# Kernel optimization log

Measured on AMD Instinct MI355X. Metric: run time of the kernel, lower is better.

## Reference

```python
import jax, jax.numpy as jnp
import numpy as np

H, W, C = 1080, 1920, 3


def setup_inputs() -> dict:
    key = jax.random.key(0)
    k1, k2, k3 = jax.random.split(key, 3)
    img = jax.random.normal(k1, (H, W, C), dtype=jnp.float32)
    # ~10px typical displacement for realistic optical flow
    flow = jax.random.normal(k2, (1, H, W, 2), dtype=jnp.float32) * 10.0
    # depths in [0.1, 80); no pixel hits the 100.0 invalid sentinel
    depth = jax.random.uniform(k3, (H, W), dtype=jnp.float32, minval=0.1, maxval=80.0)
    return {"img": img, "flow": flow, "depth": depth, "split": 10}


def reference(img, flow, depth, split):
    # Depth-ordered forward-warping splat (z-buffer style compositing).
    # kernel_size=1 -> nearest-neighbor splat: each source pixel (y,x) writes
    # its value to (round(y+flow_y), round(x+flow_x)); passes go far->near and
    # nearer (nonzero) writes overwrite farther ones.
    flow = flow[0]                      # [H, W, 2], (dx, dy)
    h, w, c = img.shape

    # midpoints of the depth histogram, excluding the 100.0 invalid sentinel
    valid = depth != 100.0
    sd = jnp.sort(jnp.where(valid, depth, jnp.inf).ravel())
    l = valid.sum()
    step = l // split
    mids = jnp.concatenate(
        [jnp.take(sd, jnp.arange(split) * step), jnp.take(sd, l - 1)[None]]
    )  # [split+1], ascending

    ys, xs = jnp.meshgrid(jnp.arange(h), jnp.arange(w), indexing="ij")
    ty = jnp.round(ys + flow[..., 1]).astype(jnp.int32)   # target row
    tx = jnp.round(xs + flow[..., 0]).astype(jnp.int32)   # target col

    res = jnp.zeros_like(img)
    for i in range(split, 0, -1):       # far bin first, near bin last
        dmask = (depth < mids[i]) & (depth >= mids[i - 1])   # [H, W]
        # pixels outside the bin scatter to row h -> dropped (mode='drop')
        ty_i = jnp.where(dmask, ty, h)
        out = jnp.zeros_like(img).at[ty_i, tx].set(
            img * dmask[..., None].astype(img.dtype), mode="drop"
        )
        # nearer nonzero splats overwrite; zeros keep previous content
        res = res * (out == 0) + out
    return res
```

## Files before the change

### kernel.cpp

```cpp
#include <hip/hip_runtime.h>

typedef unsigned int u32;

static constexpr int HH = 1080, WW = 1920;
static constexpr int NPIX = HH * WW;
static constexpr int NQ = 17;
static constexpr int MAXOWN = 16;
static constexpr int OPB = 4;
static constexpr int NGRP = MAXOWN / OPB;
static constexpr int NBLK = 512;
static constexpr int BT   = 1024;
static constexpr int R1 = 16;
static constexpr int NCH1 = 64;
static constexpr int TS = 64;
static constexpr int TCX = WW / TS;
static constexpr int TCY = (HH + TS - 1) / TS;
static constexpr int NTILE = TCX * TCY;
static constexpr int NT512 = 512;

static constexpr size_t MIDS_OFF  = 0;
static constexpr size_t QB1_OFF   = 128;
static constexpr size_t QR1_OFF   = 256;
static constexpr size_t OIDX_OFF  = 384;
static constexpr size_t OBIN_OFF  = 512;
static constexpr size_t NOWN_OFF  = 640;
static constexpr size_t KEY22_OFF = 768;
static constexpr size_t R2O_OFF   = 896;
static constexpr size_t TOT1_OFF  = 1024;
static constexpr size_t GH2_OFF   = TOT1_OFF + (size_t)R1 * 4096 * 4;
static constexpr size_t ZERO_BYTES = GH2_OFF + (size_t)NQ * 1024 * 4;
static constexpr size_t TCNT_OFF  = ZERO_BYTES;
static constexpr size_t TTOT_OFF  = TCNT_OFF + (size_t)NBLK * NT512 * 4;
static constexpr size_t TBASE_OFF = TTOT_OFF + NT512 * 4;
static constexpr size_t TEND_OFF  = TBASE_OFF + NT512 * 4;
static constexpr size_t BASE2_OFF = TEND_OFF + NT512 * 4;
static constexpr size_t GH1_OFF   = BASE2_OFF + (size_t)NBLK * NT512 * 4;
static constexpr size_t PAIRS_OFF = GH1_OFF + (size_t)MAXOWN * NCH1 * 1024 * 4;

__device__ __forceinline__ int target_of(int y, int x, float fx, float fy) {
    int ty = (int)rintf((float)y + fy);
    int tx = (int)rintf((float)x + fx);
    if (ty < 0) ty += HH;
    if (tx < 0) tx += WW;
    if ((unsigned)ty >= (unsigned)HH || (unsigned)tx >= (unsigned)WW) return -1;
    return ty * WW + tx;
}

__global__ __launch_bounds__(BT) void k_histA_cnt(const float* __restrict__ depth,
                                                  const float* __restrict__ flow,
                                                  u32* __restrict__ tot1,
                                                  u32* __restrict__ tcnt) {
    __shared__ u32 h[4096];
    __shared__ u32 tc[NT512];
    int tid = threadIdx.x;
    for (int j = tid; j < 4096; j += BT) h[j] = 0;
    for (int j = tid; j < NT512; j += BT) tc[j] = 0;
    __syncthreads();
    const int nvec = NPIX / 4;
    for (int v = blockIdx.x * BT + tid; v < nvec; v += gridDim.x * BT) {
        int i = v * 4;
        float4 d4 = ((const float4*)depth)[v];
        float4 fa = ((const float4*)flow)[v * 2];
        float4 fb = ((const float4*)flow)[v * 2 + 1];
        int y = i / WW, x0 = i - y * WW;
        float dd[4] = {d4.x, d4.y, d4.z, d4.w};
        float fx[4] = {fa.x, fa.z, fb.x, fb.z};
        float fy[4] = {fa.y, fa.w, fb.y, fb.w};
        #pragma unroll
        for (int j = 0; j < 4; ++j) {
            if (dd[j] != 100.0f)
                atomicAdd(&h[__float_as_uint(dd[j]) >> 20], 1u);
            int t = target_of(y, x0 + j, fx[j], fy[j]);
            if (t >= 0) {
                int ty = t / WW, tx = t - ty * WW;
                atomicAdd(&tc[(ty >> 6) * TCX + (tx >> 6)], 1u);
            }
        }
    }
    __syncthreads();
    u32 rep = blockIdx.x & (R1 - 1);
    for (int j = tid; j < 4096; j += BT) {
        u32 v = h[j];
        if (v) atomicAdd(&tot1[rep * 4096 + j], v);
    }
    for (int j = tid; j < NT512; j += BT)
        tcnt[blockIdx.x * NT512 + j] = tc[j];
}

__global__ __launch_bounds__(NBLK) void k_tscan(const u32* __restrict__ tcnt,
                                                u32* __restrict__ ttot,
                                                u32* __restrict__ base2) {
    __shared__ u32 s[NBLK];
    int t = blockIdx.x, b = threadIdx.x;
    u32 v = tcnt[b * NT512 + t];
    s[b] = v;
    __syncthreads();
    for (int off = 1; off < NBLK; off <<= 1) {
        u32 x = (b >= off) ? s[b - off] : 0;
        __syncthreads();
        s[b] += x;
        __syncthreads();
    }
    base2[b * NT512 + t] = s[b] - v;
    if (b == NBLK - 1) ttot[t] = s[NBLK - 1];
}

__global__ __launch_bounds__(1024) void k_selA(const u32* __restrict__ tot1,
                                               const int* __restrict__ splitp,
                                               const u32* __restrict__ ttot,
                                               u32* __restrict__ qb1, u32* __restrict__ qr1,
                                               u32* __restrict__ oidx, u32* __restrict__ obin,
                                               u32* __restrict__ nown,
                                               u32* __restrict__ tbase, u32* __restrict__ tend) {
    __shared__ u32 part[1024];
    __shared__ u32 qbS[NQ], qcS[NQ];
    __shared__ u32 totalsh;
    int tid = threadIdx.x;
    int split = *splitp;
    int base = tid * 4;
    u32 cc[4] = {0, 0, 0, 0};
    for (int r = 0; r < R1; ++r)
        for (int j = 0; j < 4; ++j) cc[j] += tot1[r * 4096 + base + j];
    u32 local = cc[0] + cc[1] + cc[2] + cc[3];
    part[tid] = local;
    __syncthreads();
    for (int off = 1; off < 1024; off <<= 1) {
        u32 v = (tid >= off) ? part[tid - off] : 0;
        __syncthreads();
        part[tid] += v;
        __syncthreads();
    }
    if (tid == 1023) totalsh = part[1023];
    __syncthreads();
    u32 l = totalsh;
    u32 step = l / (u32)split;
    u32 cum = part[tid] - local;
    for (int j = 0; j < 4; ++j) {
        u32 c = cc[j];
        if (c) {
            for (int q = 0; q <= split; ++q) {
                u32 r = (q < split) ? (u32)q * step : l - 1u;
                if (r >= cum && r < cum + c) {
                    qb1[q] = (u32)(base + j);
                    qr1[q] = r - cum;
                    qbS[q] = (u32)(base + j);
                    qcS[q] = c;
                }
            }
        }
        cum += c;
    }
    __syncthreads();
    if (tid == 0) {
        int w = -1;
        u32 prev = 0xFFFFFFFFu;
        for (int q = 0; q <= split; ++q) {
            if (qbS[q] != prev) { ++w; prev = qbS[q]; obin[w] = qbS[q]; }
            oidx[q] = (u32)w;
        }
        for (int w2 = w + 1; w2 < MAXOWN; ++w2) obin[w2] = 0xFFFFFFFFu;
        *nown = (u32)(w + 1);
    }
    __syncthreads();
    u32 tv = (tid < NT512) ? ttot[tid] : 0;
    part[tid] = tv;
    __syncthreads();
    for (int off = 1; off < 1024; off <<= 1) {
        u32 v = (tid >= off) ? part[tid - off] : 0;
        __syncthreads();
        part[tid] += v;
        __syncthreads();
    }
    if (tid < NT512) {
        tbase[tid] = part[tid] - tv;
        tend[tid]  = part[tid];
    }
}

__global__ __launch_bounds__(1024) void k_ph1(const float* __restrict__ depth,
                                              const u32* __restrict__ obin,
                                              const u32* __restrict__ nownp,
                                              u32* __restrict__ ghist) {
    int c = blockIdx.x / NGRP;
    int g = blockIdx.x % NGRP;
    int w0 = g * OPB;
    int nown = (int)*nownp;
    if (w0 >= nown) return;
    __shared__ u32 h[OPB * 1024];
    int tid = threadIdx.x;
    u32 ob[OPB];
    #pragma unroll
    for (int k = 0; k < OPB; ++k)
        ob[k] = (w0 + k < nown) ? obin[w0 + k] : 0xFFFFFFFFu;
    for (int j = tid; j < OPB * 1024; j += 1024) h[j] = 0;
    __syncthreads();
    const int per = (NPIX / 4) / NCH1;
    int lo = c * per, hi = lo + per;
    for (int v = lo + tid; v < hi; v += 1024) {
        float4 d4 = ((const float4*)depth)[v];
        float dd[4] = {d4.x, d4.y, d4.z, d4.w};
        #pragma unroll
        for (int j = 0; j < 4; ++j) {
            u32 bits = __float_as_uint(dd[j]);
            u32 b1 = bits >> 20;
            #pragma unroll
            for (int k = 0; k < OPB; ++k)
                if (ob[k] == b1)
                    atomicAdd(&h[k * 1024 + ((bits >> 10) & 1023u)], 1u);
        }
    }
    __syncthreads();
    for (int j = tid; j < OPB * 1024; j += 1024) {
        int k = j >> 10, bin = j & 1023;
        int w = w0 + k;
        if (w < nown) ghist[(w * NCH1 + c) * 1024 + bin] = h[j];
    }
}

__global__ __launch_bounds__(1024) void k_red1(const int* __restrict__ splitp,
                                               const u32* __restrict__ qb1,
                                               const u32* __restrict__ qr1,
                                               const u32* __restrict__ oidx,
                                               const u32* __restrict__ ghist,
                                               u32* __restrict__ key22, u32* __restrict__ r2o) {
    int q = blockIdx.x;
    if (q > *splitp) return;
    int w = (int)oidx[q];
    __shared__ u32 part[1024];
    int tid = threadIdx.x;
    u32 local = 0;
    for (int c = 0; c < NCH1; ++c) local += ghist[(w * NCH1 + c) * 1024 + tid];
    part[tid] = local;
    __syncthreads();
    for (int off = 1; off < 1024; off <<= 1) {
        u32 v = (tid >= off) ? part[tid - off] : 0;
        __syncthreads();
        part[tid] += v;
        __syncthreads();
    }
    u32 target = qr1[q];
    u32 cum = part[tid] - local;
    if (local && target >= cum && target < cum + local) {
        key22[q] = (qb1[q] << 10) | (u32)tid;
        r2o[q] = target - cum;
    }
}

__global__ __launch_bounds__(256) void k_ph2(const float* __restrict__ depth,
                                             const int* __restrict__ splitp,
                                             const u32* __restrict__ key22,
                                             u32* __restrict__ gh2) {
    __shared__ u32 k22[NQ];
    int tid = threadIdx.x, split = *splitp;
    if (tid < NQ) k22[tid] = (tid <= split) ? key22[tid] : 0xFFFFFFFFu;
    __syncthreads();
    const int nvec = NPIX / 4;
    for (int v = blockIdx.x * blockDim.x + tid; v < nvec; v += gridDim.x * blockDim.x) {
        float4 d4 = ((const float4*)depth)[v];
        float dd[4] = {d4.x, d4.y, d4.z, d4.w};
        #pragma unroll
        for (int j = 0; j < 4; ++j) {
            if (dd[j] != 100.0f) {
                u32 bits = __float_as_uint(dd[j]);
                u32 hi22 = bits >> 10;
                for (int q = 0; q <= split; ++q)
                    if (k22[q] == hi22) atomicAdd(&gh2[q * 1024 + (bits & 1023u)], 1u);
            }
        }
    }
}

__global__ __launch_bounds__(1024) void k_red2(const int* __restrict__ splitp,
                                               const u32* __restrict__ key22,
                                               const u32* __restrict__ r2o,
                                               const u32* __restrict__ gh2,
                                               float* __restrict__ mids) {
    int q = blockIdx.x;
    if (q > *splitp) return;
    __shared__ u32 part[1024];
    int tid = threadIdx.x;
    u32 local = gh2[q * 1024 + tid];
    part[tid] = local;
    __syncthreads();
    for (int off = 1; off < 1024; off <<= 1) {
        u32 v = (tid >= off) ? part[tid - off] : 0;
        __syncthreads();
        part[tid] += v;
        __syncthreads();
    }
    u32 target = r2o[q];
    u32 cum = part[tid] - local;
    if (local && target >= cum && target < cum + local)
        mids[q] = __uint_as_float((key22[q] << 10) | (u32)tid);
}

__global__ __launch_bounds__(BT) void k_scatter(const float* __restrict__ depth,
                                                const float* __restrict__ flow,
                                                const int* __restrict__ splitp,
                                                const float* __restrict__ mids,
                                                const u32* __restrict__ tbase,
                                                const u32* __restrict__ base2,
                                                uint2* __restrict__ pairs) {
    __shared__ u32 cur[NT512];
    __shared__ float msh[NQ];
    int tid = threadIdx.x, split = *splitp;
    if (tid < NQ) msh[tid] = (tid <= split) ? mids[tid] : 0.f;
    for (int j = tid; j < NT512; j += BT)
        cur[j] = tbase[j] + base2[blockIdx.x * NT512 + j];
    __syncthreads();
    const int nvec = NPIX / 4;
    for (int v = blockIdx.x * BT + tid; v < nvec; v += gridDim.x * BT) {
        int i = v * 4;
        float4 d4 = ((const float4*)depth)[v];
        float4 fa = ((const float4*)flow)[v * 2];
        float4 fb = ((const float4*)flow)[v * 2 + 1];
        int y = i / WW, x0 = i - y * WW;
        float dd[4] = {d4.x, d4.y, d4.z, d4.w};
        float fx[4] = {fa.x, fa.z, fb.x, fb.z};
        float fy[4] = {fa.y, fa.w, fb.y, fb.w};
        #pragma unroll
        for (int j = 0; j < 4; ++j) {
            int t = target_of(y, x0 + j, fx[j], fy[j]);
            if (t < 0) continue;
            float d = dd[j];
            int rank = -1;
            for (int k = 1; k <= split; ++k)
                if (d >= msh[k - 1] && d < msh[k]) { rank = split - k; break; }
            u32 p = (rank >= 0) ? (u32)rank * (u32)NPIX + (u32)(i + j) + 1u : 0u;
            int ty = t / WW, tx = t - ty * WW;
            int tile = (ty >> 6) * TCX + (tx >> 6);
            u32 pos = atomicAdd(&cur[tile], 1u);
            pairs[pos] = make_uint2((u32)t, p);
        }
    }
}

__global__ __launch_bounds__(1024) void k_tile_reduce(const uint2* __restrict__ pairs,
                                                      const u32* __restrict__ tbase,
                                                      const u32* __restrict__ tend,
                                                      const float* __restrict__ img,
                                                      float* __restrict__ out) {
    __shared__ u32 zb[TS * TS];
    int tid = threadIdx.x;
    int tile = blockIdx.x;
    for (int c = tid; c < TS * TS; c += 1024) zb[c] = 0;
    __syncthreads();
    int ty0 = (tile / TCX) << 6, tx0 = (tile % TCX) << 6;
    u32 b = tbase[tile], e = tend[tile];
    for (u32 k = b + tid; k < e; k += 1024) {
        uint2 pr = pairs[k];
        int t = (int)pr.x;
        int ty = t / WW, tx = t - ty * WW;
        atomicMax(&zb[((ty - ty0) << 6) | (tx - tx0)], pr.y);
    }
    __syncthreads();
    for (int c = tid; c < TS * TS; c += 1024) {
        int ty = ty0 + (c >> 6);
        if (ty >= HH) continue;
        int tx = tx0 + (c & 63);
        u32 p = zb[c];
        float r = 0.f, g = 0.f, bl = 0.f;
        if (p) {
            u32 src = (p - 1u) % (u32)NPIX;
            r  = img[src * 3 + 0];
            g  = img[src * 3 + 1];
            bl = img[src * 3 + 2];
        }
        int t = ty * WW + tx;
        out[t * 3 + 0] = r;
        out[t * 3 + 1] = g;
        out[t * 3 + 2] = bl;
    }
}

extern "C" void kernel_launch(void* const* d_in, const int* in_sizes, int n_in,
                              void* d_out, int out_size, void* d_ws, size_t ws_size,
                              hipStream_t stream) {
    const float* img    = (const float*)d_in[0];
    const float* flow   = (const float*)d_in[1];
    const float* depth  = (const float*)d_in[2];
    const int*   splitp = (const int*)d_in[3];

    char* ws = (char*)d_ws;
    float* mids  = (float*)(ws + MIDS_OFF);
    u32*   qb1   = (u32*)(ws + QB1_OFF);
    u32*   qr1   = (u32*)(ws + QR1_OFF);
    u32*   oidx  = (u32*)(ws + OIDX_OFF);
    u32*   obin  = (u32*)(ws + OBIN_OFF);
    u32*   nown  = (u32*)(ws + NOWN_OFF);
    u32*   key22 = (u32*)(ws + KEY22_OFF);
    u32*   r2o   = (u32*)(ws + R2O_OFF);
    u32*   tot1  = (u32*)(ws + TOT1_OFF);
    u32*   gh2   = (u32*)(ws + GH2_OFF);
    u32*   tcnt  = (u32*)(ws + TCNT_OFF);
    u32*   ttot  = (u32*)(ws + TTOT_OFF);
    u32*   tbase = (u32*)(ws + TBASE_OFF);
    u32*   tend  = (u32*)(ws + TEND_OFF);
    u32*   base2 = (u32*)(ws + BASE2_OFF);
    u32*   gh1   = (u32*)(ws + GH1_OFF);
    uint2* pairs = (uint2*)(ws + PAIRS_OFF);
    float* out   = (float*)d_out;

    hipMemsetAsync(d_ws, 0, ZERO_BYTES, stream);

    k_histA_cnt  <<<NBLK, BT, 0, stream>>>(depth, flow, tot1, tcnt);
    k_tscan      <<<NT512, NBLK, 0, stream>>>(tcnt, ttot, base2);
    k_selA       <<<1, 1024, 0, stream>>>(tot1, splitp, ttot, qb1, qr1, oidx, obin, nown, tbase, tend);
    k_ph1        <<<NCH1 * NGRP, 1024, 0, stream>>>(depth, obin, nown, gh1);
    k_red1       <<<NQ, 1024, 0, stream>>>(splitp, qb1, qr1, oidx, gh1, key22, r2o);
    k_ph2        <<<2048, 256, 0, stream>>>(depth, splitp, key22, gh2);
    k_red2       <<<NQ, 1024, 0, stream>>>(splitp, key22, r2o, gh2, mids);
    k_scatter    <<<NBLK, BT, 0, stream>>>(depth, flow, splitp, mids, tbase, base2, pairs);
    k_tile_reduce<<<NTILE, 1024, 0, stream>>>(pairs, tbase, tend, img, out);
}
```

Measured before the change: 96.92 us.

## Fuse quantile selection kernels into one cooperative kernel with grid syncs

Replaces the memset and seven small launches (histogram, tile scan, selection, two-level radix refinement) with a single cooperative kernel of 256 blocks using grid.sync between phases. It also halves the block count for the tile-count and scatter decomposition to 256 contiguous chunks. The aim is to remove launch gaps and serialization overhead between many tiny kernels. In exchange, parallelism in each phase is capped at 256x512 threads, grid-wide barriers add their own cost, and phases such as the single-block selection run while the rest of the grid idles.

```diff
diff --git a/kernel.cpp b/kernel.cpp
--- a/kernel.cpp
+++ b/kernel.cpp
@@ -1,21 +1,24 @@
 #include <hip/hip_runtime.h>
-
+#include <hip/hip_cooperative_groups.h>
+
+namespace cg = cooperative_groups;
 typedef unsigned int u32;
 
 static constexpr int HH = 1080, WW = 1920;
 static constexpr int NPIX = HH * WW;
+static constexpr int NVEC = NPIX / 4;
 static constexpr int NQ = 17;
 static constexpr int MAXOWN = 16;
+static constexpr int NBC = 256;
+static constexpr int BTC = 512;
+static constexpr int CHUNK = NVEC / NBC;
+static constexpr int R1 = 16;
 static constexpr int OPB = 4;
-static constexpr int NGRP = MAXOWN / OPB;
-static constexpr int NBLK = 512;
-static constexpr int BT   = 1024;
-static constexpr int R1 = 16;
 static constexpr int NCH1 = 64;
+static constexpr int CH1V = NVEC / NCH1;
 static constexpr int TS = 64;
 static constexpr int TCX = WW / TS;
-static constexpr int TCY = (HH + TS - 1) / TS;
-static constexpr int NTILE = TCX * TCY;
+static constexpr int NTILE = 510;
 static constexpr int NT512 = 512;
 
 static constexpr size_t MIDS_OFF  = 0;
@@ -26,15 +29,15 @@
 static constexpr size_t NOWN_OFF  = 640;
 static constexpr size_t KEY22_OFF = 768;
 static constexpr size_t R2O_OFF   = 896;
-static constexpr size_t TOT1_OFF  = 1024;
+static constexpr size_t TTOT_OFF  = 1024;
+static constexpr size_t TBASE_OFF = 3072;
+static constexpr size_t TEND_OFF  = 5120;
+static constexpr size_t TOT1_OFF  = 8192;
 static constexpr size_t GH2_OFF   = TOT1_OFF + (size_t)R1 * 4096 * 4;
-static constexpr size_t ZERO_BYTES = GH2_OFF + (size_t)NQ * 1024 * 4;
-static constexpr size_t TCNT_OFF  = ZERO_BYTES;
-static constexpr size_t TTOT_OFF  = TCNT_OFF + (size_t)NBLK * NT512 * 4;
-static constexpr size_t TBASE_OFF = TTOT_OFF + NT512 * 4;
-static constexpr size_t TEND_OFF  = TBASE_OFF + NT512 * 4;
-static constexpr size_t BASE2_OFF = TEND_OFF + NT512 * 4;
-static constexpr size_t GH1_OFF   = BASE2_OFF + (size_t)NBLK * NT512 * 4;
+static constexpr size_t ZCNT      = (R1 * 4096 + NQ * 1024);
+static constexpr size_t TCNT_OFF  = GH2_OFF + (size_t)NQ * 1024 * 4;
+static constexpr size_t BASE2_OFF = TCNT_OFF + (size_t)NBC * NT512 * 4;
+static constexpr size_t GH1_OFF   = BASE2_OFF + (size_t)NBC * NT512 * 4;
 static constexpr size_t PAIRS_OFF = GH1_OFF + (size_t)MAXOWN * NCH1 * 1024 * 4;
 
 __device__ __forceinline__ int target_of(int y, int x, float fx, float fy) {
@@ -46,270 +49,286 @@
     return ty * WW + tx;
 }
 
-__global__ __launch_bounds__(BT) void k_histA_cnt(const float* __restrict__ depth,
-                                                  const float* __restrict__ flow,
-                                                  u32* __restrict__ tot1,
-                                                  u32* __restrict__ tcnt) {
-    __shared__ u32 h[4096];
-    __shared__ u32 tc[NT512];
-    int tid = threadIdx.x;
-    for (int j = tid; j < 4096; j += BT) h[j] = 0;
-    for (int j = tid; j < NT512; j += BT) tc[j] = 0;
-    __syncthreads();
-    const int nvec = NPIX / 4;
-    for (int v = blockIdx.x * BT + tid; v < nvec; v += gridDim.x * BT) {
-        int i = v * 4;
-        float4 d4 = ((const float4*)depth)[v];
-        float4 fa = ((const float4*)flow)[v * 2];
-        float4 fb = ((const float4*)flow)[v * 2 + 1];
-        int y = i / WW, x0 = i - y * WW;
-        float dd[4] = {d4.x, d4.y, d4.z, d4.w};
-        float fx[4] = {fa.x, fa.z, fb.x, fb.z};
-        float fy[4] = {fa.y, fa.w, fb.y, fb.w};
+__global__ __launch_bounds__(BTC) void k_quant(const float* __restrict__ depth,
+                                               const float* __restrict__ flow,
+                                               const int* __restrict__ splitp,
+                                               char* __restrict__ ws) {
+    cg::grid_group grid = cg::this_grid();
+    __shared__ u32 SM[4608];
+    __shared__ u32 SMQ[40];
+
+    float* mids  = (float*)(ws + MIDS_OFF);
+    u32* qb1   = (u32*)(ws + QB1_OFF);
+    u32* qr1   = (u32*)(ws + QR1_OFF);
+    u32* oidx  = (u32*)(ws + OIDX_OFF);
+    u32* obin  = (u32*)(ws + OBIN_OFF);
+    u32* nown  = (u32*)(ws + NOWN_OFF);
+    u32* key22 = (u32*)(ws + KEY22_OFF);
+    u32* r2o   = (u32*)(ws + R2O_OFF);
+    u32* ttot  = (u32*)(ws + TTOT_OFF);
+    u32* tbase = (u32*)(ws + TBASE_OFF);
+    u32* tend  = (u32*)(ws + TEND_OFF);
+    u32* tot1  = (u32*)(ws + TOT1_OFF);
+    u32* gh2   = (u32*)(ws + GH2_OFF);
+    u32* tcnt  = (u32*)(ws + TCNT_OFF);
+    u32* base2 = (u32*)(ws + BASE2_OFF);
+    u32* gh1   = (u32*)(ws + GH1_OFF);
+
+    const int b = blockIdx.x, tid = threadIdx.x;
+    const int split = *splitp;
+
+    {
+        u32* z = tot1;
+        for (int j = b * BTC + tid; j < (int)ZCNT; j += NBC * BTC) z[j] = 0;
+    }
+    grid.sync();
+
+    {
+        u32* h  = SM;
+        u32* tc = SM + 4096;
+        for (int j = tid; j < 4096; j += BTC) h[j] = 0;
+        tc[tid] = 0;
+        __syncthreads();
+        int lo = b * CHUNK;
+        for (int v = lo + tid; v < lo + CHUNK; v += BTC) {
+            int i = v * 4;
+            float4 d4 = ((const float4*)depth)[v];
+            float4 fa = ((const float4*)flow)[v * 2];
+            float4 fb = ((const float4*)flow)[v * 2 + 1];
+            int y = i / WW, x0 = i - y * WW;
+            float dd[4] = {d4.x, d4.y, d4.z, d4.w};
+            float fx[4] = {fa.x, fa.z, fb.x, fb.z};
+            float fy[4] = {fa.y, fa.w, fb.y, fb.w};
+            #pragma unroll
+            for (int j = 0; j < 4; ++j) {
+                if (dd[j] != 100.0f)
+                    atomicAdd(&h[__float_as_uint(dd[j]) >> 20], 1u);
+                int t = target_of(y, x0 + j, fx[j], fy[j]);
+                if (t >= 0) {
+                    int ty = t / WW, tx = t - ty * WW;
+                    atomicAdd(&tc[(ty >> 6) * TCX + (tx >> 6)], 1u);
+                }
+            }
+        }
+        __syncthreads();
+        u32 rep = (u32)(b & (R1 - 1));
+        for (int j = tid; j < 4096; j += BTC) {
+            u32 v = h[j];
+            if (v) atomicAdd(&tot1[rep * 4096 + j], v);
+        }
+        tcnt[b * NT512 + tid] = tc[tid];
+    }
+    grid.sync();
+
+    {
+        int j = tid & 255, half = tid >> 8;
+        int t = 2 * b + half;
+        u32 val = tcnt[j * NT512 + t];
+        u32* s = SM;
+        s[tid] = val;
+        __syncthreads();
+        for (int off = 1; off < 256; off <<= 1) {
+            u32 x = (j >= off) ? s[tid - off] : 0;
+            __syncthreads();
+            s[tid] += x;
+            __syncthreads();
+        }
+        base2[j * NT512 + t] = s[tid] - val;
+        if (j == 255) ttot[t] = s[tid];
+    }
+    if (b == 0) {
+        __syncthreads();
+        u32* part = SM;
+        u32* qbS  = SMQ;
+        int base = tid * 8;
+        u32 cc[8];
         #pragma unroll
-        for (int j = 0; j < 4; ++j) {
-            if (dd[j] != 100.0f)
-                atomicAdd(&h[__float_as_uint(dd[j]) >> 20], 1u);
-            int t = target_of(y, x0 + j, fx[j], fy[j]);
-            if (t >= 0) {
-                int ty = t / WW, tx = t - ty * WW;
-                atomicAdd(&tc[(ty >> 6) * TCX + (tx >> 6)], 1u);
-            }
-        }
-    }
-    __syncthreads();
-    u32 rep = blockIdx.x & (R1 - 1);
-    for (int j = tid; j < 4096; j += BT) {
-        u32 v = h[j];
-        if (v) atomicAdd(&tot1[rep * 4096 + j], v);
-    }
-    for (int j = tid; j < NT512; j += BT)
-        tcnt[blockIdx.x * NT512 + j] = tc[j];
-}
-
-__global__ __launch_bounds__(NBLK) void k_tscan(const u32* __restrict__ tcnt,
-                                                u32* __restrict__ ttot,
-                                                u32* __restrict__ base2) {
-    __shared__ u32 s[NBLK];
-    int t = blockIdx.x, b = threadIdx.x;
-    u32 v = tcnt[b * NT512 + t];
-    s[b] = v;
-    __syncthreads();
-    for (int off = 1; off < NBLK; off <<= 1) {
-        u32 x = (b >= off) ? s[b - off] : 0;
-        __syncthreads();
-        s[b] += x;
-        __syncthreads();
-    }
-    base2[b * NT512 + t] = s[b] - v;
-    if (b == NBLK - 1) ttot[t] = s[NBLK - 1];
-}
-
-__global__ __launch_bounds__(1024) void k_selA(const u32* __restrict__ tot1,
-                                               const int* __restrict__ splitp,
-                                               const u32* __restrict__ ttot,
-                                               u32* __restrict__ qb1, u32* __restrict__ qr1,
-                                               u32* __restrict__ oidx, u32* __restrict__ obin,
-                                               u32* __restrict__ nown,
-                                               u32* __restrict__ tbase, u32* __restrict__ tend) {
-    __shared__ u32 part[1024];
-    __shared__ u32 qbS[NQ], qcS[NQ];
-    __shared__ u32 totalsh;
-    int tid = threadIdx.x;
-    int split = *splitp;
-    int base = tid * 4;
-    u32 cc[4] = {0, 0, 0, 0};
-    for (int r = 0; r < R1; ++r)
-        for (int j = 0; j < 4; ++j) cc[j] += tot1[r * 4096 + base + j];
-    u32 local = cc[0] + cc[1] + cc[2] + cc[3];
-    part[tid] = local;
-    __syncthreads();
-    for (int off = 1; off < 1024; off <<= 1) {
-        u32 v = (tid >= off) ? part[tid - off] : 0;
-        __syncthreads();
-        part[tid] += v;
-        __syncthreads();
-    }
-    if (tid == 1023) totalsh = part[1023];
-    __syncthreads();
-    u32 l = totalsh;
-    u32 step = l / (u32)split;
-    u32 cum = part[tid] - local;
-    for (int j = 0; j < 4; ++j) {
-        u32 c = cc[j];
-        if (c) {
+        for (int k = 0; k < 8; ++k) cc[k] = 0;
+        for (int r = 0; r < R1; ++r) {
+            const u32* tp = tot1 + r * 4096 + base;
+            #pragma unroll
+            for (int k = 0; k < 8; ++k) cc[k] += tp[k];
+        }
+        u32 local = 0;
+        #pragma unroll
+        for (int k = 0; k < 8; ++k) local += cc[k];
+        part[tid] = local;
+        __syncthreads();
+        for (int off = 1; off < BTC; off <<= 1) {
+            u32 x = (tid >= off) ? part[tid - off] : 0;
+            __syncthreads();
+            part[tid] += x;
+            __syncthreads();
+        }
+        if (tid == BTC - 1) SMQ[32] = part[BTC - 1];
+        __syncthreads();
+        u32 l = SMQ[32];
+        u32 step = l / (u32)split;
+        u32 cum = part[tid] - local;
+        for (int k = 0; k < 8; ++k) {
+            u32 c = cc[k];
+            if (c) {
+                for (int q = 0; q <= split; ++q) {
+                    u32 r = (q < split) ? (u32)q * step : l - 1u;
+                    if (r >= cum && r < cum + c) {
+                        qb1[q] = (u32)(base + k);
+                        qr1[q] = r - cum;
+                        qbS[q] = (u32)(base + k);
+                    }
+                }
+            }
+            cum += c;
+        }
+        __syncthreads();
+        if (tid == 0) {
+            int w = -1;
+            u32 prev = 0xFFFFFFFFu;
             for (int q = 0; q <= split; ++q) {
-                u32 r = (q < split) ? (u32)q * step : l - 1u;
-                if (r >= cum && r < cum + c) {
-                    qb1[q] = (u32)(base + j);
-                    qr1[q] = r - cum;
-                    qbS[q] = (u32)(base + j);
-                    qcS[q] = c;
-                }
-            }
-        }
-        cum += c;
-    }
-    __syncthreads();
-    if (tid == 0) {
-        int w = -1;
-        u32 prev = 0xFFFFFFFFu;
-        for (int q = 0; q <= split; ++q) {
-            if (qbS[q] != prev) { ++w; prev = qbS[q]; obin[w] = qbS[q]; }
-            oidx[q] = (u32)w;
-        }
-        for (int w2 = w + 1; w2 < MAXOWN; ++w2) obin[w2] = 0xFFFFFFFFu;
-        *nown = (u32)(w + 1);
-    }
-    __syncthreads();
-    u32 tv = (tid < NT512) ? ttot[tid] : 0;
-    part[tid] = tv;
-    __syncthreads();
-    for (int off = 1; off < 1024; off <<= 1) {
-        u32 v = (tid >= off) ? part[tid - off] : 0;
-        __syncthreads();
-        part[tid] += v;
-        __syncthreads();
-    }
-    if (tid < NT512) {
-        tbase[tid] = part[tid] - tv;
-        tend[tid]  = part[tid];
-    }
-}
-
-__global__ __launch_bounds__(1024) void k_ph1(const float* __restrict__ depth,
-                                              const u32* __restrict__ obin,
-                                              const u32* __restrict__ nownp,
-                                              u32* __restrict__ ghist) {
-    int c = blockIdx.x / NGRP;
-    int g = blockIdx.x % NGRP;
-    int w0 = g * OPB;
-    int nown = (int)*nownp;
-    if (w0 >= nown) return;
-    __shared__ u32 h[OPB * 1024];
-    int tid = threadIdx.x;
-    u32 ob[OPB];
-    #pragma unroll
-    for (int k = 0; k < OPB; ++k)
-        ob[k] = (w0 + k < nown) ? obin[w0 + k] : 0xFFFFFFFFu;
-    for (int j = tid; j < OPB * 1024; j += 1024) h[j] = 0;
-    __syncthreads();
-    const int per = (NPIX / 4) / NCH1;
-    int lo = c * per, hi = lo + per;
-    for (int v = lo + tid; v < hi; v += 1024) {
-        float4 d4 = ((const float4*)depth)[v];
-        float dd[4] = {d4.x, d4.y, d4.z, d4.w};
-        #pragma unroll
-        for (int j = 0; j < 4; ++j) {
-            u32 bits = __float_as_uint(dd[j]);
-            u32 b1 = bits >> 20;
+                if (qbS[q] != prev) { ++w; prev = qbS[q]; obin[w] = qbS[q]; }
+                oidx[q] = (u32)w;
+            }
+            for (int w2 = w + 1; w2 < MAXOWN; ++w2) obin[w2] = 0xFFFFFFFFu;
+            *nown = (u32)(w + 1);
+        }
+    }
+    grid.sync();
+
+    {
+        int c2 = b >> 2, g = b & 3, w0 = g * OPB;
+        int nw = (int)*nown;
+        if (w0 < nw) {
+            u32 ob[OPB];
             #pragma unroll
             for (int k = 0; k < OPB; ++k)
-                if (ob[k] == b1)
-                    atomicAdd(&h[k * 1024 + ((bits >> 10) & 1023u)], 1u);
-        }
-    }
-    __syncthreads();
-    for (int j = tid; j < OPB * 1024; j += 1024) {
-        int k = j >> 10, bin = j & 1023;
-        int w = w0 + k;
-        if (w < nown) ghist[(w * NCH1 + c) * 1024 + bin] = h[j];
+                ob[k] = (w0 + k < nw) ? obin[w0 + k] : 0xFFFFFFFFu;
+            u32* h = SM;
+            for (int j = tid; j < 4096; j += BTC) h[j] = 0;
+            __syncthreads();
+            int lo = c2 * CH1V;
+            for (int v = lo + tid; v < lo + CH1V; v += BTC) {
+                float4 d4 = ((const float4*)depth)[v];
+                float dd[4] = {d4.x, d4.y, d4.z, d4.w};
+                #pragma unroll
+                for (int j = 0; j < 4; ++j) {
+                    u32 bits = __float_as_uint(dd[j]);
+                    u32 b1 = bits >> 20;
+                    #pragma unroll
+                    for (int k = 0; k < OPB; ++k)
+                        if (ob[k] == b1)
+                            atomicAdd(&h[k * 1024 + ((bits >> 10) & 1023u)], 1u);
+                }
+            }
+            __syncthreads();
+            for (int j = tid; j < 4096; j += BTC) {
+                int k = j >> 10, w = w0 + k;
+                if (w < nw) gh1[(w * NCH1 + c2) * 1024 + (j & 1023)] = SM[j];
+            }
+        }
+        if (b == NBC - 1) {
+            __syncthreads();
+            u32* s = SM;
+            u32 tv = ttot[tid];
+            s[tid] = tv;
+            __syncthreads();
+            for (int off = 1; off < BTC; off <<= 1) {
+                u32 x = (tid >= off) ? s[tid - off] : 0;
+                __syncthreads();
+                s[tid] += x;
+                __syncthreads();
+            }
+            tbase[tid] = s[tid] - tv;
+            tend[tid]  = s[tid];
+        }
+    }
+    grid.sync();
+
+    if (b <= split) {
+        int w = (int)oidx[b];
+        u32 l0 = 0, l1 = 0;
+        for (int c = 0; c < NCH1; ++c) {
+            const u32* gp = gh1 + (size_t)(w * NCH1 + c) * 1024 + 2 * tid;
+            l0 += gp[0];
+            l1 += gp[1];
+        }
+        u32* part = SM;
+        u32 loc = l0 + l1;
+        part[tid] = loc;
+        __syncthreads();
+        for (int off = 1; off < BTC; off <<= 1) {
+            u32 x = (tid >= off) ? part[tid - off] : 0;
+            __syncthreads();
+            part[tid] += x;
+            __syncthreads();
+        }
+        u32 target = qr1[b];
+        u32 cum = part[tid] - loc;
+        if (l0 && target >= cum && target < cum + l0) {
+            key22[b] = (qb1[b] << 10) | (u32)(2 * tid);
+            r2o[b] = target - cum;
+        } else if (l1 && target >= cum + l0 && target < cum + loc) {
+            key22[b] = (qb1[b] << 10) | (u32)(2 * tid + 1);
+            r2o[b] = target - cum - l0;
+        }
+    }
+    grid.sync();
+
+    {
+        u32* k22 = SMQ;
+        if (tid < NQ) k22[tid] = (tid <= split) ? key22[tid] : 0xFFFFFFFFu;
+        __syncthreads();
+        int lo = b * CHUNK;
+        for (int v = lo + tid; v < lo + CHUNK; v += BTC) {
+            float4 d4 = ((const float4*)depth)[v];
+            float dd[4] = {d4.x, d4.y, d4.z, d4.w};
+            #pragma unroll
+            for (int j = 0; j < 4; ++j) {
+                if (dd[j] != 100.0f) {
+                    u32 bits = __float_as_uint(dd[j]);
+                    u32 hi22 = bits >> 10;
+                    for (int q = 0; q <= split; ++q)
+                        if (k22[q] == hi22) atomicAdd(&gh2[q * 1024 + (bits & 1023u)], 1u);
+                }
+            }
+        }
+    }
+    grid.sync();
+
+    if (b <= split) {
+        u32 l0 = gh2[b * 1024 + 2 * tid], l1 = gh2[b * 1024 + 2 * tid + 1];
+        u32* part = SM;
+        u32 loc = l0 + l1;
+        part[tid] = loc;
+        __syncthreads();
+        for (int off = 1; off < BTC; off <<= 1) {
+            u32 x = (tid >= off) ? part[tid - off] : 0;
+            __syncthreads();
+            part[tid] += x;
+            __syncthreads();
+        }
+        u32 target = r2o[b];
+        u32 cum = part[tid] - loc;
+        if (l0 && target >= cum && target < cum + l0)
+            mids[b] = __uint_as_float((key22[b] << 10) | (u32)(2 * tid));
+        else if (l1 && target >= cum + l0 && target < cum + loc)
+            mids[b] = __uint_as_float((key22[b] << 10) | (u32)(2 * tid + 1));
     }
 }
 
-__global__ __launch_bounds__(1024) void k_red1(const int* __restrict__ splitp,
-                                               const u32* __restrict__ qb1,
-                                               const u32* __restrict__ qr1,
-                                               const u32* __restrict__ oidx,
-                                               const u32* __restrict__ ghist,
-                                               u32* __restrict__ key22, u32* __restrict__ r2o) {
-    int q = blockIdx.x;
-    if (q > *splitp) return;
-    int w = (int)oidx[q];
-    __shared__ u32 part[1024];
-    int tid = threadIdx.x;
-    u32 local = 0;
-    for (int c = 0; c < NCH1; ++c) local += ghist[(w * NCH1 + c) * 1024 + tid];
-    part[tid] = local;
-    __syncthreads();
-    for (int off = 1; off < 1024; off <<= 1) {
-        u32 v = (tid >= off) ? part[tid - off] : 0;
-        __syncthreads();
-        part[tid] += v;
-        __syncthreads();
-    }
-    u32 target = qr1[q];
-    u32 cum = part[tid] - local;
-    if (local && target >= cum && target < cum + local) {
-        key22[q] = (qb1[q] << 10) | (u32)tid;
-        r2o[q] = target - cum;
-    }
-}
-
-__global__ __launch_bounds__(256) void k_ph2(const float* __restrict__ depth,
-                                             const int* __restrict__ splitp,
-                                             const u32* __restrict__ key22,
-                                             u32* __restrict__ gh2) {
-    __shared__ u32 k22[NQ];
-    int tid = threadIdx.x, split = *splitp;
-    if (tid < NQ) k22[tid] = (tid <= split) ? key22[tid] : 0xFFFFFFFFu;
-    __syncthreads();
-    const int nvec = NPIX / 4;
-    for (int v = blockIdx.x * blockDim.x + tid; v < nvec; v += gridDim.x * blockDim.x) {
-        float4 d4 = ((const float4*)depth)[v];
-        float dd[4] = {d4.x, d4.y, d4.z, d4.w};
-        #pragma unroll
-        for (int j = 0; j < 4; ++j) {
-            if (dd[j] != 100.0f) {
-                u32 bits = __float_as_uint(dd[j]);
-                u32 hi22 = bits >> 10;
-                for (int q = 0; q <= split; ++q)
-                    if (k22[q] == hi22) atomicAdd(&gh2[q * 1024 + (bits & 1023u)], 1u);
-            }
-        }
-    }
-}
-
-__global__ __launch_bounds__(1024) void k_red2(const int* __restrict__ splitp,
-                                               const u32* __restrict__ key22,
-                                               const u32* __restrict__ r2o,
-                                               const u32* __restrict__ gh2,
-                                               float* __restrict__ mids) {
-    int q = blockIdx.x;
-    if (q > *splitp) return;
-    __shared__ u32 part[1024];
-    int tid = threadIdx.x;
-    u32 local = gh2[q * 1024 + tid];
-    part[tid] = local;
-    __syncthreads();
-    for (int off = 1; off < 1024; off <<= 1) {
-        u32 v = (tid >= off) ? part[tid - off] : 0;
-        __syncthreads();
-        part[tid] += v;
-        __syncthreads();
-    }
-    u32 target = r2o[q];
-    u32 cum = part[tid] - local;
-    if (local && target >= cum && target < cum + local)
-        mids[q] = __uint_as_float((key22[q] << 10) | (u32)tid);
-}
-
-__global__ __launch_bounds__(BT) void k_scatter(const float* __restrict__ depth,
-                                                const float* __restrict__ flow,
-                                                const int* __restrict__ splitp,
-                                                const float* __restrict__ mids,
-                                                const u32* __restrict__ tbase,
-                                                const u32* __restrict__ base2,
-                                                uint2* __restrict__ pairs) {
+__global__ __launch_bounds__(1024) void k_scatter(const float* __restrict__ depth,
+                                                  const float* __restrict__ flow,
+                                                  const int* __restrict__ splitp,
+                                                  const float* __restrict__ mids,
+                                                  const u32* __restrict__ tbase,
+                                                  const u32* __restrict__ base2,
+                                                  uint2* __restrict__ pairs) {
     __shared__ u32 cur[NT512];
     __shared__ float msh[NQ];
-    int tid = threadIdx.x, split = *splitp;
+    int tid = threadIdx.x, c = blockIdx.x, split = *splitp;
     if (tid < NQ) msh[tid] = (tid <= split) ? mids[tid] : 0.f;
-    for (int j = tid; j < NT512; j += BT)
-        cur[j] = tbase[j] + base2[blockIdx.x * NT512 + j];
+    if (tid < NT512) cur[tid] = tbase[tid] + base2[c * NT512 + tid];
     __syncthreads();
-    const int nvec = NPIX / 4;
-    for (int v = blockIdx.x * BT + tid; v < nvec; v += gridDim.x * BT) {
+    int lo = c * CHUNK;
+    for (int v = lo + tid; v < lo + CHUNK; v += 1024) {
         int i = v * 4;
         float4 d4 = ((const float4*)depth)[v];
         float4 fa = ((const float4*)flow)[v * 2];
@@ -383,33 +402,15 @@
 
     char* ws = (char*)d_ws;
     float* mids  = (float*)(ws + MIDS_OFF);
-    u32*   qb1   = (u32*)(ws + QB1_OFF);
-    u32*   qr1   = (u32*)(ws + QR1_OFF);
-    u32*   oidx  = (u32*)(ws + OIDX_OFF);
-    u32*   obin  = (u32*)(ws + OBIN_OFF);
-    u32*   nown  = (u32*)(ws + NOWN_OFF);
-    u32*   key22 = (u32*)(ws + KEY22_OFF);
-    u32*   r2o   = (u32*)(ws + R2O_OFF);
-    u32*   tot1  = (u32*)(ws + TOT1_OFF);
-    u32*   gh2   = (u32*)(ws + GH2_OFF);
-    u32*   tcnt  = (u32*)(ws + TCNT_OFF);
-    u32*   ttot  = (u32*)(ws + TTOT_OFF);
     u32*   tbase = (u32*)(ws + TBASE_OFF);
     u32*   tend  = (u32*)(ws + TEND_OFF);
     u32*   base2 = (u32*)(ws + BASE2_OFF);
-    u32*   gh1   = (u32*)(ws + GH1_OFF);
     uint2* pairs = (uint2*)(ws + PAIRS_OFF);
     float* out   = (float*)d_out;
 
-    hipMemsetAsync(d_ws, 0, ZERO_BYTES, stream);
-
-    k_histA_cnt  <<<NBLK, BT, 0, stream>>>(depth, flow, tot1, tcnt);
-    k_tscan      <<<NT512, NBLK, 0, stream>>>(tcnt, ttot, base2);
-    k_selA       <<<1, 1024, 0, stream>>>(tot1, splitp, ttot, qb1, qr1, oidx, obin, nown, tbase, tend);
-    k_ph1        <<<NCH1 * NGRP, 1024, 0, stream>>>(depth, obin, nown, gh1);
-    k_red1       <<<NQ, 1024, 0, stream>>>(splitp, qb1, qr1, oidx, gh1, key22, r2o);
-    k_ph2        <<<2048, 256, 0, stream>>>(depth, splitp, key22, gh2);
-    k_red2       <<<NQ, 1024, 0, stream>>>(splitp, key22, r2o, gh2, mids);
-    k_scatter    <<<NBLK, BT, 0, stream>>>(depth, flow, splitp, mids, tbase, base2, pairs);
+    void* args[] = {(void*)&depth, (void*)&flow, (void*)&splitp, (void*)&ws};
+    hipLaunchCooperativeKernel((const void*)k_quant, dim3(NBC), dim3(BTC), args, 0, stream);
+
+    k_scatter    <<<NBC, 1024, 0, stream>>>(depth, flow, splitp, mids, tbase, base2, pairs);
     k_tile_reduce<<<NTILE, 1024, 0, stream>>>(pairs, tbase, tend, img, out);
 }
```

New measurement: 259.2 us. +167.4%, slower.
